# Optimization experiments

Hardware: AMD Instinct MI355X
Metric: run time of the kernel (lower is better)

## Reference

```python
import jax, jax.numpy as jnp
import numpy as np

B, C_IN, H, W = 32, 3, 256, 256
PATCH = 16
E, C_OUT = 8, 8
C_PROJ = 16
NUM_CLASSES = 1000
SPP_LEVELS = (1, 2, 4)
GATE_STEEPNESS = 10.0


def _conv(x, w, b, pad):
    # x: [N,C,H,W], w: [O,C,kh,kw]
    y = jax.lax.conv_general_dilated(x, w, (1, 1), [(pad, pad), (pad, pad)],
                                     dimension_numbers=('NCHW', 'OIHW', 'NCHW'))
    return y + b[None, :, None, None]


def _forward(X, expert_w, expert_b, proj_w, proj_b, keys, threshold,
             final_w, final_b, lin_w, lin_b):
    Bx, C, Hx, Wx = X.shape
    h, w = Hx // PATCH, Wx // PATCH
    P = h * w
    # 1) patch extraction: [B,C,H,W] -> [B*P, C, ph, pw]
    xp = (X.reshape(Bx, C, h, PATCH, w, PATCH)
           .transpose(0, 2, 4, 1, 3, 5)
           .reshape(Bx * P, C, PATCH, PATCH))
    # 2) router: conv projection -> global avg pool -> key similarity -> softmax -> soft threshold gate
    proj = _conv(xp, proj_w, proj_b, 1)                 # [BP, 16, ph, pw]
    pooled = proj.mean(axis=(2, 3))                     # [BP, 16]
    scores = jax.nn.softmax(pooled @ keys.T, axis=-1)   # [BP, E]
    gate = scores * jax.nn.sigmoid((scores - threshold) * GATE_STEEPNESS)
    gate = gate / (gate.sum(axis=-1, keepdims=True) + 1e-9)
    gate = gate.reshape(Bx, P, E)
    # 3) all experts fused as one conv with E*C_OUT output channels (conv3x3 pad1 + ReLU)
    ew = expert_w.reshape(E * C_OUT, C, 3, 3)
    eb = expert_b.reshape(E * C_OUT)
    outs = jax.nn.relu(_conv(xp, ew, eb, 1))            # [BP, E*Cout, ph, pw]
    outs = outs.reshape(Bx, P, E, C_OUT, PATCH, PATCH)
    # 4) router-weighted combine over experts
    comb = jnp.einsum('bpe,bpeclm->bpclm', gate, outs)  # [B,P,Cout,ph,pw]
    # 5) reassemble patches -> [B, Cout, H, W]
    y = (comb.reshape(Bx, h, w, C_OUT, PATCH, PATCH)
             .transpose(0, 3, 1, 4, 2, 5)
             .reshape(Bx, C_OUT, h * PATCH, w * PATCH))
    # 6) final 1x1 conv with padding=4 (zero-pad input, bias added everywhere)
    ypad = jnp.pad(y, ((0, 0), (0, 0), (4, 4), (4, 4)))
    y = jnp.einsum('oc,bchw->bohw', final_w[:, :, 0, 0], ypad) + final_b[None, :, None, None]
    # 7) spatial pyramid pooling (levels 1,2,4) -> [B, Cout*21]
    Bc, Cc, Hc, Wc = y.shape
    feats = [y.reshape(Bc, Cc, l, Hc // l, l, Wc // l).mean(axis=(3, 5)).reshape(Bc, -1)
             for l in SPP_LEVELS]
    spp = jnp.concatenate(feats, axis=-1)
    # 8) classification head
    return spp @ lin_w + lin_b


def setup_inputs() -> dict:
    key = jax.random.key(0)
    ks = jax.random.split(key, 11)
    s = 0.1
    spp_dim = C_OUT * sum(l * l for l in SPP_LEVELS)  # 168
    return {
        'X': jax.random.normal(ks[0], (B, C_IN, H, W), jnp.float32),
        'expert_w': jax.random.normal(ks[1], (E, C_OUT, C_IN, 3, 3), jnp.float32) * s,
        'expert_b': jax.random.normal(ks[2], (E, C_OUT), jnp.float32) * s,
        'proj_w': jax.random.normal(ks[3], (C_PROJ, C_IN, 3, 3), jnp.float32) * s,
        'proj_b': jax.random.normal(ks[4], (C_PROJ,), jnp.float32) * s,
        'keys': jax.random.normal(ks[5], (E, C_PROJ), jnp.float32) * s,
        'threshold': jnp.array(0.125, jnp.float32),
        'final_w': jax.random.normal(ks[6], (C_OUT, C_OUT, 1, 1), jnp.float32) * s,
        'final_b': jax.random.normal(ks[7], (C_OUT,), jnp.float32) * s,
        'lin_w': jax.random.normal(ks[8], (spp_dim, NUM_CLASSES), jnp.float32) * s,
        'lin_b': jax.random.normal(ks[9], (NUM_CLASSES,), jnp.float32) * s,
    }


def reference(X, expert_w, expert_b, proj_w, proj_b, keys, threshold,
              final_w, final_b, lin_w, lin_b):
    return _forward(X, expert_w, expert_b, proj_w, proj_b, keys, threshold,
                    final_w, final_b, lin_w, lin_b)
```

## Files before the change

### kernel.cpp

```cpp
#include <hip/hip_runtime.h>
#include <hip/hip_bf16.h>
#include <math.h>


typedef short bf16x8 __attribute__((ext_vector_type(8)));
typedef float f32x4 __attribute__((ext_vector_type(4)));
typedef float pf2 __attribute__((ext_vector_type(2)));

__device__ __forceinline__ int cellOf(int r) {
    int rr = r + 4;
    return (rr >= 66) + (rr >= 132) + (rr >= 198);
}

__device__ __forceinline__ unsigned int packbf2(float lo, float hi) {
    __hip_bfloat162 h = __float22bfloat162_rn(make_float2(lo, hi));
    unsigned int u;
    __builtin_memcpy(&u, &h, 4);
    return u;
}

__global__ __launch_bounds__(256) void prep_kernel(
    const float* __restrict__ ew, const float* __restrict__ ebg,
    const float* __restrict__ pw, const float* __restrict__ pb,
    const float* __restrict__ keys, float* __restrict__ Sy,
    unsigned short* __restrict__ Bg, float* __restrict__ cbf)
{
    const int t = threadIdx.x;
    for (int i = t; i < 8192; i += 256) Sy[i] = 0.f;
    if (t < 72) {
        float sv[32];
        #pragma unroll
        for (int s = 0; s < 32; ++s) {
            int q, kx; bool zz = false;
            if (s < 16)       { q = s >> 1;  kx = s & 1; }
            else if (s < 18)  { q = 8;       kx = s - 16; }
            else if (s < 26)  { q = s - 18;  kx = 2; }
            else if (s == 26) { q = 8;       kx = 2; }
            else              { q = 0; kx = 0; zz = true; }
            const int ky = q / 3, c = q - ky * 3;
            const int widx = c * 9 + ky * 3 + kx;
            float a;
            if (t < 64) {
                a = ew[t * 27 + widx];
            } else {
                const int e = t - 64;
                a = 0.f;
                #pragma unroll
                for (int o = 0; o < 16; ++o)
                    a += keys[e * 16 + o] * pw[o * 27 + widx];
            }
            sv[s] = zz ? 0.f : a;
        }
        uint4 q0, q1, q2v, q3v;
        q0.x  = packbf2(sv[0],  sv[1]);  q0.y  = packbf2(sv[2],  sv[3]);
        q0.z  = packbf2(sv[4],  sv[5]);  q0.w  = packbf2(sv[6],  sv[7]);
        q1.x  = packbf2(sv[8],  sv[9]);  q1.y  = packbf2(sv[10], sv[11]);
        q1.z  = packbf2(sv[12], sv[13]); q1.w  = packbf2(sv[14], sv[15]);
        q2v.x = packbf2(sv[16], sv[17]); q2v.y = packbf2(sv[18], sv[19]);
        q2v.z = packbf2(sv[20], sv[21]); q2v.w = packbf2(sv[22], sv[23]);
        q3v.x = packbf2(sv[24], sv[25]); q3v.y = packbf2(sv[26], sv[27]);
        q3v.z = packbf2(sv[28], sv[29]); q3v.w = packbf2(sv[30], sv[31]);
        uint4* dst = reinterpret_cast<uint4*>(&Bg[t * 32]);
        dst[0] = q0; dst[1] = q1; dst[2] = q2v; dst[3] = q3v;
    }
    if (t >= 128 && t < 208) {
        const int i = t - 128;
        float c;
        if (i < 64) {
            c = ebg[i];
        } else {
            const int e = (i - 64) & 7;
            c = 0.f;
            #pragma unroll
            for (int o = 0; o < 16; ++o) c += keys[e * 16 + o] * pb[o];
        }
        cbf[i] = c;
    }
}

#define CONV_STEP(SB, ACCJ) do {                                            \
    uint4 pkv;                                                              \
    pkv.x = pkw[offp0 + (SB)];                                              \
    pkv.y = pkw[offp1 + (SB)];                                              \
    pkv.z = pkw[offp2 + (SB)];                                              \
    pkv.w = pkw[offp3 + (SB)];                                              \
    const bf16x8 afr = __builtin_bit_cast(bf16x8, pkv);                     \
    const f32x4 a0 = __builtin_amdgcn_mfma_f32_16x16x32_bf16(afr, bfr0, cbv0, 0, 0, 0); \
    const f32x4 a1 = __builtin_amdgcn_mfma_f32_16x16x32_bf16(afr, bfr1, cbv1, 0, 0, 0); \
    const f32x4 a2 = __builtin_amdgcn_mfma_f32_16x16x32_bf16(afr, bfr2, cbv2, 0, 0, 0); \
    const f32x4 a3 = __builtin_amdgcn_mfma_f32_16x16x32_bf16(afr, bfr3, cbv3, 0, 0, 0); \
    a4acc = __builtin_amdgcn_mfma_f32_16x16x32_bf16(afr, bfr4, a4acc, 0, 0, 0); \
    const pf2 z2_ = {0.f, 0.f};                                             \
    {                                                                       \
        const pf2 l_ = __builtin_elementwise_max((pf2)__builtin_shufflevector(a0, a0, 0, 1), z2_); \
        const pf2 h_ = __builtin_elementwise_max((pf2)__builtin_shufflevector(a0, a0, 2, 3), z2_); \
        pall2[0] += l_ + h_;                                                \
        if (ACCJ) psb2[0] += l_ * jm2lo + h_ * jm2hi;                       \
    }                                                                       \
    {                                                                       \
        const pf2 l_ = __builtin_elementwise_max((pf2)__builtin_shufflevector(a1, a1, 0, 1), z2_); \
        const pf2 h_ = __builtin_elementwise_max((pf2)__builtin_shufflevector(a1, a1, 2, 3), z2_); \
        pall2[1] += l_ + h_;                                                \
        if (ACCJ) psb2[1] += l_ * jm2lo + h_ * jm2hi;                       \
    }                                                                       \
    {                                                                       \
        const pf2 l_ = __builtin_elementwise_max((pf2)__builtin_shufflevector(a2, a2, 0, 1), z2_); \
        const pf2 h_ = __builtin_elementwise_max((pf2)__builtin_shufflevector(a2, a2, 2, 3), z2_); \
        pall2[2] += l_ + h_;                                                \
        if (ACCJ) psb2[2] += l_ * jm2lo + h_ * jm2hi;                       \
    }                                                                       \
    {                                                                       \
        const pf2 l_ = __builtin_elementwise_max((pf2)__builtin_shufflevector(a3, a3, 0, 1), z2_); \
        const pf2 h_ = __builtin_elementwise_max((pf2)__builtin_shufflevector(a3, a3, 2, 3), z2_); \
        pall2[3] += l_ + h_;                                                \
        if (ACCJ) psb2[3] += l_ * jm2lo + h_ * jm2hi;                       \
    }                                                                       \
} while (0)

#define GATES_FROM_RSUM()                                                   \
    rsum += __shfl_xor(rsum, 16);                                           \
    rsum += __shfl_xor(rsum, 32);                                           \
    float gv[4];                                                            \
    {                                                                       \
        float lg = rsum * (1.f / 256.f);                                    \
        float mx = fmaxf(lg, __shfl_xor(lg, 1));                            \
        mx = fmaxf(mx, __shfl_xor(mx, 2));                                  \
        mx = fmaxf(mx, __shfl_xor(mx, 4));                                  \
        float ex = __expf(lg - mx);                                         \
        float s = ex;                                                       \
        s += __shfl_xor(s, 1); s += __shfl_xor(s, 2); s += __shfl_xor(s, 4);\
        float sc = ex / s;                                                  \
        float g = sc / (1.f + __expf(-(sc - thr) * 10.f));                  \
        float gs = g;                                                       \
        gs += __shfl_xor(gs, 1); gs += __shfl_xor(gs, 2); gs += __shfl_xor(gs, 4); \
        float gn = g / (gs + 1e-9f);                                        \
        const int gb = (lid & 56);                                          \
        const int hb = (lid >> 3) & 1;                                      \
        gv[0] = __shfl(gn, gb | (0 + hb));                                  \
        gv[1] = __shfl(gn, gb | (2 + hb));                                  \
        gv[2] = __shfl(gn, gb | (4 + hb));                                  \
        gv[3] = __shfl(gn, gb | (6 + hb));                                  \
    }

__global__ __launch_bounds__(256, 4) void fused_kernel(
    const float* __restrict__ X, const unsigned short* __restrict__ Bg,
    const float* __restrict__ thr_p, const float* __restrict__ cbf,
    float* __restrict__ Sy)
{
    __shared__ __align__(16) unsigned int pk[4][1952];

    const int t = threadIdx.x;
    const int wid = t >> 6, lid = t & 63;
    const int r16 = lid & 15, kb = lid >> 4;

    const int wgid = blockIdx.x;
    const int virt = (wgid & 7) * 256 + (wgid >> 3);

    const int gp = (virt << 2) + wid;
    const int b = gp >> 8;
    const int pi = (gp >> 4) & 15, pj = gp & 15;
    const int rbase = pi << 4, cbase = pj << 4;

    unsigned int* pkw = pk[wid];
    const float thr = thr_p[0];

    const int lr = lid >> 2, lq = lid & 3;
    const float* xb = X + ((b * 3) << 16) + ((rbase + lr) << 8) + cbase + (lq << 2);
    const float4 xv0 = *reinterpret_cast<const float4*>(xb);
    const float4 xv1 = *reinterpret_cast<const float4*>(xb + 65536);
    const float4 xv2 = *reinterpret_cast<const float4*>(xb + 131072);

    const bf16x8 bfr0 = *reinterpret_cast<const bf16x8*>(&Bg[(r16) * 32 + (kb << 3)]);
    const bf16x8 bfr1 = *reinterpret_cast<const bf16x8*>(&Bg[(16 + r16) * 32 + (kb << 3)]);
    const bf16x8 bfr2 = *reinterpret_cast<const bf16x8*>(&Bg[(32 + r16) * 32 + (kb << 3)]);
    const bf16x8 bfr3 = *reinterpret_cast<const bf16x8*>(&Bg[(48 + r16) * 32 + (kb << 3)]);
    const bf16x8 bfr4 = *reinterpret_cast<const bf16x8*>(&Bg[(64 + (r16 & 7)) * 32 + (kb << 3)]);

    const float cbs0 = cbf[r16];
    const float cbs1 = cbf[16 + r16];
    const float cbs2 = cbf[32 + r16];
    const float cbs3 = cbf[48 + r16];
    const float cbs4 = cbf[64 + r16];

    {
        uint4* pk4 = reinterpret_cast<uint4*>(pkw);
        const uint4 z = make_uint4(0u, 0u, 0u, 0u);
        #pragma unroll
        for (int i = 0; i < 8; ++i) {
            const int idx = lid + (i << 6);
            if (idx < 488) pk4[idx] = z;
        }
    }
    __builtin_amdgcn_wave_barrier();

    float s0 = __shfl_up(xv0.w, 1);
    float s1 = __shfl_up(xv1.w, 1);
    float s2 = __shfl_up(xv2.w, 1);
    const float c0p = (lq == 0) ? 0.f : s0;
    const float c1p = (lq == 0) ? 0.f : s1;
    const float c2p = (lq == 0) ? 0.f : s2;
    float nxx = __shfl_down(xv0.x, 4);
    float nxy = __shfl_down(xv0.y, 4);
    float nxz = __shfl_down(xv0.z, 4);
    float nxw = __shfl_down(xv0.w, 4);
    if (lr == 15) { nxx = 0.f; nxy = 0.f; nxz = 0.f; nxw = 0.f; }

    {
        const int y = lr + 1;
        const int b2 = y * 54 + (lq << 2);
        unsigned int u0, u1, u2, u3;
        u0 = packbf2(c0p,   xv0.x); u1 = packbf2(xv0.x, xv0.y);
        u2 = packbf2(xv0.y, xv0.z); u3 = packbf2(xv0.z, xv0.w);
        *reinterpret_cast<uint2*>(&pkw[b2])      = make_uint2(u0, u1);
        *reinterpret_cast<uint2*>(&pkw[b2 + 2])  = make_uint2(u2, u3);
        u0 = packbf2(c1p,   xv1.x); u1 = packbf2(xv1.x, xv1.y);
        u2 = packbf2(xv1.y, xv1.z); u3 = packbf2(xv1.z, xv1.w);
        *reinterpret_cast<uint2*>(&pkw[b2 + 18]) = make_uint2(u0, u1);
        *reinterpret_cast<uint2*>(&pkw[b2 + 20]) = make_uint2(u2, u3);
        u0 = packbf2(c2p,   xv2.x); u1 = packbf2(xv2.x, xv2.y);
        u2 = packbf2(xv2.y, xv2.z); u3 = packbf2(xv2.z, xv2.w);
        *reinterpret_cast<uint2*>(&pkw[b2 + 36]) = make_uint2(u0, u1);
        *reinterpret_cast<uint2*>(&pkw[b2 + 38]) = make_uint2(u2, u3);

        const int bx = 976 + y * 54 + (lq << 2);
        u0 = packbf2(xv0.x, xv1.x); u1 = packbf2(xv0.y, xv1.y);
        u2 = packbf2(xv0.z, xv1.z); u3 = packbf2(xv0.w, xv1.w);
        *reinterpret_cast<uint2*>(&pkw[bx])      = make_uint2(u0, u1);
        *reinterpret_cast<uint2*>(&pkw[bx + 2])  = make_uint2(u2, u3);
        u0 = packbf2(xv1.x, xv2.x); u1 = packbf2(xv1.y, xv2.y);
        u2 = packbf2(xv1.z, xv2.z); u3 = packbf2(xv1.w, xv2.w);
        *reinterpret_cast<uint2*>(&pkw[bx + 18]) = make_uint2(u0, u1);
        *reinterpret_cast<uint2*>(&pkw[bx + 20]) = make_uint2(u2, u3);
        u0 = packbf2(xv2.x, nxx);  u1 = packbf2(xv2.y, nxy);
        u2 = packbf2(xv2.z, nxz);  u3 = packbf2(xv2.w, nxw);
        *reinterpret_cast<uint2*>(&pkw[bx + 36]) = make_uint2(u0, u1);
        *reinterpret_cast<uint2*>(&pkw[bx + 38]) = make_uint2(u2, u3);

        if (lr == 0) {
            const int b0 = 976 + 36 + (lq << 2);
            u0 = packbf2(0.f, xv0.x); u1 = packbf2(0.f, xv0.y);
            u2 = packbf2(0.f, xv0.z); u3 = packbf2(0.f, xv0.w);
            *reinterpret_cast<uint2*>(&pkw[b0])     = make_uint2(u0, u1);
            *reinterpret_cast<uint2*>(&pkw[b0 + 2]) = make_uint2(u2, u3);
        }
    }
    __builtin_amdgcn_wave_barrier();

    int offp0, offp1, offp2, offp3;
    if (kb < 2) {
        const int t0 = kb * 72 + r16;
        offp0 = t0; offp1 = t0 + 18; offp2 = t0 + 36; offp3 = t0 + 54;
    } else if (kb == 2) {
        offp0 = 144 + r16; offp1 = 977 + r16; offp2 = 1013 + r16; offp3 = 1049 + r16;
    } else {
        offp0 = 1085 + r16; offp1 = 1121 + r16; offp2 = 1121 + r16; offp3 = 1121 + r16;
    }

    const f32x4 cbv0 = {cbs0, cbs0, cbs0, cbs0};
    const f32x4 cbv1 = {cbs1, cbs1, cbs1, cbs1};
    const f32x4 cbv2 = {cbs2, cbs2, cbs2, cbs2};
    const f32x4 cbv3 = {cbs3, cbs3, cbs3, cbs3};
    const float rb16 = cbs4 * 16.f;
    f32x4 a4acc = {rb16, rb16, rb16, rb16};

    const int iA = cellOf(rbase), iB = cellOf(rbase + 15);
    const int jA = cellOf(cbase), jB = cellOf(cbase + 15);
    const int isp = (iA + 1) * 66 - 4 - rbase;
    const int jsp = (jA + 1) * 66 - 4 - cbase;
    const bool anySplit = (isp < 16) | (jsp < 16);

    const int bc16 = b << 4;
    const pf2 zz2 = {0.f, 0.f};

    if (!anySplit) {
        pf2 pall2[4] = {zz2, zz2, zz2, zz2};
        pf2 psb2[4]  = {zz2, zz2, zz2, zz2};
        pf2 jm2lo = zz2, jm2hi = zz2;
        #pragma unroll
        for (int mt = 0; mt < 16; ++mt) CONV_STEP(mt * 54, 0);

        float rsum = (a4acc[0] + a4acc[1]) + (a4acc[2] + a4acc[3]);
        GATES_FROM_RSUM();

        float tt = 0.f;
        #pragma unroll
        for (int nt = 0; nt < 4; ++nt)
            tt = fmaf(gv[nt], pall2[nt].x + pall2[nt].y, tt);
        tt += __shfl_xor(tt, 8);
        tt += __shfl_xor(tt, 16);
        tt += __shfl_xor(tt, 32);
        if (lid < 8)
            atomicAdd(&Sy[(iA * 4 + jA) * 512 + bc16 + lid], tt);
    } else {
        float jmask[4];
        #pragma unroll
        for (int r = 0; r < 4; ++r)
            jmask[r] = ((kb << 2) + r >= jsp) ? 1.f : 0.f;
        const pf2 jm2lo = {jmask[0], jmask[1]};
        const pf2 jm2hi = {jmask[2], jmask[3]};

        pf2 pall2[4] = {zz2, zz2, zz2, zz2};
        pf2 psb2[4]  = {zz2, zz2, zz2, zz2};
        const int m1 = isp < 16 ? isp : 16;

        int sb = 0;
        for (int mt = 0; mt < m1; ++mt) { CONV_STEP(sb, 1); sb += 54; }
        const float pa0_0 = pall2[0].x + pall2[0].y;
        const float pa0_1 = pall2[1].x + pall2[1].y;
        const float pa0_2 = pall2[2].x + pall2[2].y;
        const float pa0_3 = pall2[3].x + pall2[3].y;
        const float pb0_0 = psb2[0].x + psb2[0].y;
        const float pb0_1 = psb2[1].x + psb2[1].y;
        const float pb0_2 = psb2[2].x + psb2[2].y;
        const float pb0_3 = psb2[3].x + psb2[3].y;
        pall2[0] = pall2[1] = pall2[2] = pall2[3] = zz2;
        psb2[0] = psb2[1] = psb2[2] = psb2[3] = zz2;
        for (int mt = m1; mt < 16; ++mt) { CONV_STEP(sb, 1); sb += 54; }

        float rsum = (a4acc[0] + a4acc[1]) + (a4acc[2] + a4acc[3]);
        GATES_FROM_RSUM();

        float tTA = gv[0] * pa0_0 + gv[1] * pa0_1 + gv[2] * pa0_2 + gv[3] * pa0_3;
        float tTB = gv[0] * pb0_0 + gv[1] * pb0_1 + gv[2] * pb0_2 + gv[3] * pb0_3;
        float tBA = 0.f, tBB = 0.f;
        #pragma unroll
        for (int nt = 0; nt < 4; ++nt) {
            tBA = fmaf(gv[nt], pall2[nt].x + pall2[nt].y, tBA);
            tBB = fmaf(gv[nt], psb2[nt].x + psb2[nt].y, tBB);
        }
        #pragma unroll
        for (int m = 8; m <= 32; m <<= 1) {
            tTA += __shfl_xor(tTA, m);
            tTB += __shfl_xor(tTB, m);
            tBA += __shfl_xor(tBA, m);
            tBB += __shfl_xor(tBB, m);
        }
        if (lid < 8) {
            atomicAdd(&Sy[(iA * 4 + jA) * 512 + bc16 + lid], tTA - tTB);
            atomicAdd(&Sy[(iA * 4 + jB) * 512 + bc16 + lid], tTB);
            atomicAdd(&Sy[(iB * 4 + jA) * 512 + bc16 + lid], tBA - tBB);
            atomicAdd(&Sy[(iB * 4 + jB) * 512 + bc16 + lid], tBB);
        }
    }
}

__global__ __launch_bounds__(256) void head_kernel(
    const float* __restrict__ Sy, const float* __restrict__ fw,
    const float* __restrict__ fb, const float* __restrict__ lw,
    const float* __restrict__ lb, float* __restrict__ out)
{
    __shared__ float syl[128];
    __shared__ float s2[32];
    __shared__ float stot[8];
    __shared__ float spp[168];
    const int t = threadIdx.x;
    const int b = blockIdx.y;
    if (t < 128) syl[t] = Sy[(t & 15) * 512 + b * 16 + (t >> 4)];
    __syncthreads();
    if (t < 32) {
        int c = t >> 2, I = (t >> 1) & 1, J = t & 1;
        const float* p = &syl[c * 16];
        s2[t] = p[(2 * I) * 4 + 2 * J] + p[(2 * I) * 4 + 2 * J + 1] +
                p[(2 * I + 1) * 4 + 2 * J] + p[(2 * I + 1) * 4 + 2 * J + 1];
    } else if (t >= 32 && t < 40) {
        int c = t - 32;
        float s = 0.f;
        #pragma unroll
        for (int i2 = 0; i2 < 16; ++i2) s += syl[c * 16 + i2];
        stot[c] = s;
    }
    __syncthreads();
    if (t < 168) {
        float acc = 0.f;
        int o;
        if (t < 8) {
            o = t;
            #pragma unroll
            for (int c = 0; c < 8; ++c) acc += fw[o * 8 + c] * stot[c];
            acc *= (1.f / 69696.f);
        } else if (t < 40) {
            int m = t - 8; o = m >> 2; int q = m & 3;
            #pragma unroll
            for (int c = 0; c < 8; ++c) acc += fw[o * 8 + c] * s2[c * 4 + q];
            acc *= (1.f / 17424.f);
        } else {
            int m = t - 40; o = m >> 4; int cell = m & 15;
            #pragma unroll
            for (int c = 0; c < 8; ++c) acc += fw[o * 8 + c] * syl[c * 16 + cell];
            acc *= (1.f / 4356.f);
        }
        spp[t] = acc + fb[o];
    }
    __syncthreads();
    const int n = blockIdx.x * 256 + t;
    if (n < 1000) {
        float acc = lb[n];
        for (int k = 0; k < 168; ++k) acc = fmaf(spp[k], lw[k * 1000 + n], acc);
        out[b * 1000 + n] = acc;
    }
}

extern "C" void kernel_launch(void* const* d_in, const int* in_sizes, int n_in,
                              void* d_out, int out_size, void* d_ws, size_t ws_size,
                              hipStream_t stream) {
    const float* X    = (const float*)d_in[0];
    const float* ew   = (const float*)d_in[1];
    const float* eb   = (const float*)d_in[2];
    const float* pw   = (const float*)d_in[3];
    const float* pb   = (const float*)d_in[4];
    const float* keys = (const float*)d_in[5];
    const float* thr  = (const float*)d_in[6];
    const float* fw   = (const float*)d_in[7];
    const float* fb   = (const float*)d_in[8];
    const float* lw   = (const float*)d_in[9];
    const float* lb   = (const float*)d_in[10];
    float* out = (float*)d_out;
    float* Sy  = (float*)d_ws;
    unsigned short* Bg = (unsigned short*)((float*)d_ws + 8192);
    float* cbf = (float*)d_ws + 9344;

    prep_kernel<<<1, 256, 0, stream>>>(ew, eb, pw, pb, keys, Sy, Bg, cbf);
    fused_kernel<<<2048, 256, 0, stream>>>(X, Bg, thr, cbf, Sy);
    head_kernel<<<dim3(4, 32), 256, 0, stream>>>(Sy, fw, fb, lw, lb, out);
}
```

Measured before the change: 37.70 us.

## Replace global atomic accumulation with per-patch partial stores reduced in head kernel

Each wave now writes its per-patch partial sums as a float4 to a dedicated slot instead of issuing atomicAdds into a shared 16-cell accumulator. The head kernel gathers and reduces those partials per SPP cell, so prep no longer has to zero the accumulator. The aim is to remove atomic contention and serialisation, in exchange for a larger workspace and more reads in the head kernel. It also raises wave priority with s_setprio around the MFMA conv loop.

```diff
diff --git a/kernel.cpp b/kernel.cpp
--- a/kernel.cpp
+++ b/kernel.cpp
@@ -22,11 +22,10 @@
 __global__ __launch_bounds__(256) void prep_kernel(
     const float* __restrict__ ew, const float* __restrict__ ebg,
     const float* __restrict__ pw, const float* __restrict__ pb,
-    const float* __restrict__ keys, float* __restrict__ Sy,
+    const float* __restrict__ keys,
     unsigned short* __restrict__ Bg, float* __restrict__ cbf)
 {
     const int t = threadIdx.x;
-    for (int i = t; i < 8192; i += 256) Sy[i] = 0.f;
     if (t < 72) {
         float sv[32];
         #pragma unroll
@@ -145,7 +144,7 @@
 __global__ __launch_bounds__(256, 4) void fused_kernel(
     const float* __restrict__ X, const unsigned short* __restrict__ Bg,
     const float* __restrict__ thr_p, const float* __restrict__ cbf,
-    float* __restrict__ Sy)
+    float* __restrict__ Sout)
 {
     __shared__ __align__(16) unsigned int pk[4][1952];
 
@@ -269,15 +268,17 @@
     const int jsp = (jA + 1) * 66 - 4 - cbase;
     const bool anySplit = (isp < 16) | (jsp < 16);
 
-    const int bc16 = b << 4;
     const pf2 zz2 = {0.f, 0.f};
 
     if (!anySplit) {
         pf2 pall2[4] = {zz2, zz2, zz2, zz2};
         pf2 psb2[4]  = {zz2, zz2, zz2, zz2};
         pf2 jm2lo = zz2, jm2hi = zz2;
+        (void)psb2; (void)jm2lo; (void)jm2hi;
+        __builtin_amdgcn_s_setprio(1);
         #pragma unroll
         for (int mt = 0; mt < 16; ++mt) CONV_STEP(mt * 54, 0);
+        __builtin_amdgcn_s_setprio(0);
 
         float rsum = (a4acc[0] + a4acc[1]) + (a4acc[2] + a4acc[3]);
         GATES_FROM_RSUM();
@@ -289,8 +290,10 @@
         tt += __shfl_xor(tt, 8);
         tt += __shfl_xor(tt, 16);
         tt += __shfl_xor(tt, 32);
-        if (lid < 8)
-            atomicAdd(&Sy[(iA * 4 + jA) * 512 + bc16 + lid], tt);
+        if (lid < 8) {
+            float4 v = make_float4(tt, 0.f, 0.f, 0.f);
+            *reinterpret_cast<float4*>(&Sout[(gp << 5) + (lid << 2)]) = v;
+        }
     } else {
         float jmask[4];
         #pragma unroll
@@ -303,6 +306,7 @@
         pf2 psb2[4]  = {zz2, zz2, zz2, zz2};
         const int m1 = isp < 16 ? isp : 16;
 
+        __builtin_amdgcn_s_setprio(1);
         int sb = 0;
         for (int mt = 0; mt < m1; ++mt) { CONV_STEP(sb, 1); sb += 54; }
         const float pa0_0 = pall2[0].x + pall2[0].y;
@@ -316,6 +320,7 @@
         pall2[0] = pall2[1] = pall2[2] = pall2[3] = zz2;
         psb2[0] = psb2[1] = psb2[2] = psb2[3] = zz2;
         for (int mt = m1; mt < 16; ++mt) { CONV_STEP(sb, 1); sb += 54; }
+        __builtin_amdgcn_s_setprio(0);
 
         float rsum = (a4acc[0] + a4acc[1]) + (a4acc[2] + a4acc[3]);
         GATES_FROM_RSUM();
@@ -336,16 +341,14 @@
             tBB += __shfl_xor(tBB, m);
         }
         if (lid < 8) {
-            atomicAdd(&Sy[(iA * 4 + jA) * 512 + bc16 + lid], tTA - tTB);
-            atomicAdd(&Sy[(iA * 4 + jB) * 512 + bc16 + lid], tTB);
-            atomicAdd(&Sy[(iB * 4 + jA) * 512 + bc16 + lid], tBA - tBB);
-            atomicAdd(&Sy[(iB * 4 + jB) * 512 + bc16 + lid], tBB);
+            float4 v = make_float4(tTA, tTB, tBA, tBB);
+            *reinterpret_cast<float4*>(&Sout[(gp << 5) + (lid << 2)]) = v;
         }
     }
 }
 
 __global__ __launch_bounds__(256) void head_kernel(
-    const float* __restrict__ Sy, const float* __restrict__ fw,
+    const float* __restrict__ Sout, const float* __restrict__ fw,
     const float* __restrict__ fb, const float* __restrict__ lw,
     const float* __restrict__ lb, float* __restrict__ out)
 {
@@ -355,8 +358,40 @@
     __shared__ float spp[168];
     const int t = threadIdx.x;
     const int b = blockIdx.y;
-    if (t < 128) syl[t] = Sy[(t & 15) * 512 + b * 16 + (t >> 4)];
+
+    if (t < 128) {
+        const int c = t & 7;
+        const int cell = t >> 3;
+        const int ci = cell >> 2, cj = cell & 3;
+        const int piLo = (ci == 0) ? 0 : (66 * ci - 4) / 16;
+        const int piHi = min(15, (66 * ci + 61) / 16);
+        const int pjLo = (cj == 0) ? 0 : (66 * cj - 4) / 16;
+        const int pjHi = min(15, (66 * cj + 61) / 16);
+        float acc = 0.f;
+        for (int pi = piLo; pi <= piHi; ++pi) {
+            const int iA = cellOf(pi << 4), iB = cellOf((pi << 4) + 15);
+            const bool ia = (iA == ci), ib = (iB == ci);
+            for (int pj = pjLo; pj <= pjHi; ++pj) {
+                const int jA = cellOf(pj << 4), jB = cellOf((pj << 4) + 15);
+                const int p = (pi << 4) | pj;
+                const float4 v = *reinterpret_cast<const float4*>(
+                    &Sout[(((b << 8) + p) << 5) + (c << 2)]);
+                float val = 0.f;
+                if (ia) {
+                    if (jA == cj) val += v.x - v.y;
+                    if (jB == cj) val += v.y;
+                }
+                if (ib) {
+                    if (jA == cj) val += v.z - v.w;
+                    if (jB == cj) val += v.w;
+                }
+                acc += val;
+            }
+        }
+        syl[c * 16 + cell] = acc;
+    }
     __syncthreads();
+
     if (t < 32) {
         int c = t >> 2, I = (t >> 1) & 1, J = t & 1;
         const float* p = &syl[c * 16];
@@ -414,12 +449,12 @@
     const float* fb   = (const float*)d_in[8];
     const float* lw   = (const float*)d_in[9];
     const float* lb   = (const float*)d_in[10];
-    float* out = (float*)d_out;
-    float* Sy  = (float*)d_ws;
-    unsigned short* Bg = (unsigned short*)((float*)d_ws + 8192);
-    float* cbf = (float*)d_ws + 9344;
-
-    prep_kernel<<<1, 256, 0, stream>>>(ew, eb, pw, pb, keys, Sy, Bg, cbf);
-    fused_kernel<<<2048, 256, 0, stream>>>(X, Bg, thr, cbf, Sy);
-    head_kernel<<<dim3(4, 32), 256, 0, stream>>>(Sy, fw, fb, lw, lb, out);
-}
+    float* out  = (float*)d_out;
+    float* Sout = (float*)d_ws;
+    unsigned short* Bg = (unsigned short*)((float*)d_ws + 262144);
+    float* cbf = (float*)d_ws + 262144 + 1152;
+
+    prep_kernel<<<1, 256, 0, stream>>>(ew, eb, pw, pb, keys, Bg, cbf);
+    fused_kernel<<<2048, 256, 0, stream>>>(X, Bg, thr, cbf, Sout);
+    head_kernel<<<dim3(4, 32), 256, 0, stream>>>(Sout, fw, fb, lw, lb, out);
+}
```

Measured after the change: 47.49 us. +26.0%, slower.
